# Optimization experiments

Hardware: AMD Instinct MI355X
Metric: run time of the kernel (lower is better)

The kernel has to match this reference:

```python
import jax, jax.numpy as jnp
import numpy as np

N_NODES = 200000


def _gcn_conv(x, W, b, src, dst, n):
    # PyG GCNConv: h = D^{-1/2} (A + I) D^{-1/2} (x @ W) + b
    h = x @ W  # [N, F_out]
    deg = jax.ops.segment_sum(jnp.ones(dst.shape[0], x.dtype), dst, num_segments=n)
    dinv = jnp.where(deg > 0, jax.lax.rsqrt(deg), 0.0)  # deg_inv_sqrt, inf -> 0
    norm = dinv[src] * dinv[dst]  # [E+N]
    msg = h[src] * norm[:, None]  # gather + scale, dominant memory traffic
    out = jax.ops.segment_sum(msg, dst, num_segments=n)
    return out + b


def setup_inputs() -> dict:
    key = jax.random.key(0)
    k1, k2, k3, k4, k5, k6 = jax.random.split(key, 6)
    x = jax.random.normal(k1, (N_NODES, 1), dtype=jnp.float32)
    edge_index = jax.random.randint(k2, (2, 12800000), 0, N_NODES, dtype=jnp.int64)
    # Glorot-style init like PyG GCNConv
    W1 = jax.random.normal(k3, (1, 16), dtype=jnp.float32) * (1.0 / np.sqrt(1))
    b1 = jnp.zeros((16,), dtype=jnp.float32)
    W2 = jax.random.normal(k4, (16, 1), dtype=jnp.float32) * (1.0 / np.sqrt(16))
    b2 = jnp.zeros((1,), dtype=jnp.float32)
    return {"x": x, "edge_index": edge_index, "W1": W1, "b1": b1, "W2": W2, "b2": b2}


def reference(x, edge_index, W1, b1, W2, b2):
    n = x.shape[0]
    # add self-loops once (static edge count: E + N)
    loops = jnp.arange(n, dtype=edge_index.dtype)
    src = jnp.concatenate([edge_index[0], loops])
    dst = jnp.concatenate([edge_index[1], loops])
    h = _gcn_conv(x, W1, b1, src, dst, n)
    h = jax.nn.relu(h)
    out = _gcn_conv(h, W2, b2, src, dst, n)
    return out
```

## Files before the change

kernel.cpp:

```cpp
#include <hip/hip_runtime.h>

#define TPB 256
#define BTPB 1024
#define STPB 512
#define LOG_S 13
#define S (1 << LOG_S)
#define RMAX 32
#define CHUNK 8192
#define MAXC 40
#define SLACK 32768
#define SCALEF 2097152.0f
#define INV_SCALEF (1.0f / 2097152.0f)


__global__ void k_initcur(int* __restrict__ cur, int R, int cap) {
    int t = threadIdx.x;
    if (t < R) cur[t] = t * cap;
}

__device__ inline int mbcnt64(unsigned long long m) {
    return __builtin_amdgcn_mbcnt_hi((unsigned)(m >> 32),
           __builtin_amdgcn_mbcnt_lo((unsigned)m, 0u));
}

__global__ __launch_bounds__(BTPB) void k_bin(const int* __restrict__ dst,
                                              const int* __restrict__ src, int e,
                                              int R, int cap,
                                              int* __restrict__ cur,
                                              unsigned* __restrict__ bkt) {
    __shared__ unsigned stage[CHUNK];
    __shared__ int h[RMAX], lofs[RMAX + 1], gbase[RMAX];
    int t = threadIdx.x;
    int b0 = blockIdx.x * CHUNK;
    int m = min(CHUNK, e - b0);
    if (t < RMAX) h[t] = 0;
    __syncthreads();
    unsigned pack[8];
    int rr[8];
    const int4* d4p = (const int4*)(dst + b0);
    const int4* s4p = (const int4*)(src + b0);
    int m4 = m >> 2;
    #pragma unroll
    for (int g = 0; g < 2; g++) {
        int i4 = g * BTPB + t;
        bool act = i4 < m4;
        int4 d = make_int4(0, 0, 0, 0), s = make_int4(0, 0, 0, 0);
        if (act) { d = d4p[i4]; s = s4p[i4]; }
        #pragma unroll
        for (int k = 0; k < 4; k++) {
            int dd = (k == 0) ? d.x : (k == 1) ? d.y : (k == 2) ? d.z : d.w;
            int ss = (k == 0) ? s.x : (k == 1) ? s.y : (k == 2) ? s.z : s.w;
            int r = act ? (dd >> LOG_S) : 31;
            unsigned long long m64 = ~0ull;
            #pragma unroll
            for (int b = 0; b < 5; b++) {
                unsigned long long vb = __ballot((r >> b) & 1);
                m64 &= ((r >> b) & 1) ? vb : ~vb;
            }
            int intra = mbcnt64(m64);
            int leader = __ffsll((long long)m64) - 1;
            int base = 0;
            if (intra == 0) base = atomicAdd(&h[r], __popcll(m64));
            base = __shfl(base, leader);
            int rk = base + intra;
            pack[g * 4 + k] = ((unsigned)(dd - (r << LOG_S)) << 18) | (unsigned)ss;
            rr[g * 4 + k] = act ? ((r << 13) | rk) : -1;
        }
    }
    __syncthreads();
    if (t < 64) {
        int hv = (t < R) ? h[t] : 0;
        int v = hv;
        for (int o = 1; o < 64; o <<= 1) {
            int u = __shfl_up(v, o);
            if (t >= o) v += u;
        }
        if (t < R) lofs[t] = v - hv;
        if (t == R - 1) lofs[R] = v;
        if (t < R && hv > 0) gbase[t] = atomicAdd(&cur[t], hv);
    }
    __syncthreads();
    #pragma unroll
    for (int k = 0; k < 8; k++) {
        if (rr[k] >= 0)
            stage[lofs[rr[k] >> 13] + (rr[k] & 8191)] = pack[k];
    }
    __syncthreads();
    for (int j = t; j < m; j += BTPB) {
        int lo = 0, hi = R;
        while (hi - lo > 1) {
            int mid = (lo + hi) >> 1;
            if (lofs[mid] <= j) lo = mid; else hi = mid;
        }
        int gi = gbase[lo] + (j - lofs[lo]);
        if (gi < (lo + 1) * cap)
            bkt[gi] = stage[j];
    }
}

template <int MODE>
__global__ __launch_bounds__(STPB) void k_scat(const unsigned* __restrict__ bkt,
                                               const int* __restrict__ cur,
                                               int cap,
                                               const float* __restrict__ val,
                                               int* __restrict__ partials, int bpr) {
    __shared__ int acc[S];
    int t = threadIdx.x;
    int r = blockIdx.x / bpr;
    int c = blockIdx.x - r * bpr;
    int4* acc4 = (int4*)acc;
    for (int j = t; j < S / 4; j += STPB) acc4[j] = make_int4(0, 0, 0, 0);
    __syncthreads();
    const unsigned* bk = bkt + (size_t)r * cap;
    int len = min(cur[r] - r * cap, cap);
    int len4 = len >> 2;
    const uint4* bk4 = (const uint4*)bk;
    int stride = bpr * STPB;
    int i0 = c * STPB + t;
    int i1 = i0 + stride;
    bool h0 = i0 < len4, h1 = i1 < len4;
    uint4 p0, p1;
    if (h0) p0 = bk4[i0];
    if (h1) p1 = bk4[i1];
    int inext = i0 + 2 * stride;
    while (h0) {
        uint4 p2;
        bool h2 = inext < len4;
        if (h2) p2 = bk4[inext];
        if (MODE == 0) {
            atomicAdd(&acc[p0.x >> 18], 1);
            atomicAdd(&acc[p0.y >> 18], 1);
            atomicAdd(&acc[p0.z >> 18], 1);
            atomicAdd(&acc[p0.w >> 18], 1);
        } else {
            atomicAdd(&acc[p0.x >> 18], (int)rintf(val[p0.x & 0x3FFFFu] * SCALEF));
            atomicAdd(&acc[p0.y >> 18], (int)rintf(val[p0.y & 0x3FFFFu] * SCALEF));
            atomicAdd(&acc[p0.z >> 18], (int)rintf(val[p0.z & 0x3FFFFu] * SCALEF));
            atomicAdd(&acc[p0.w >> 18], (int)rintf(val[p0.w & 0x3FFFFu] * SCALEF));
        }
        p0 = p1; h0 = h1;
        p1 = p2; h1 = h2;
        inext += stride;
    }
    for (int k = (len4 << 2) + c * STPB + t; k < len; k += stride) {
        unsigned p = bk[k];
        if (MODE == 0) atomicAdd(&acc[p >> 18], 1);
        else atomicAdd(&acc[p >> 18], (int)rintf(val[p & 0x3FFFFu] * SCALEF));
    }
    __syncthreads();
    int4* out4 = (int4*)(partials + (size_t)blockIdx.x * S);
    for (int j = t; j < S / 4; j += STPB) out4[j] = acc4[j];
}

__device__ inline int redp(const int* __restrict__ partials, int i, int bpr) {
    int r = i >> LOG_S;
    int slot = i & (S - 1);
    const int* p = partials + (size_t)r * bpr * S + slot;
    int s = 0;
    #pragma unroll 8
    for (int c = 0; c < bpr; c++) s += p[(size_t)c * S];
    return s;
}

__global__ void k_red_dinv(const int* __restrict__ partials, int bpr,
                           const float* __restrict__ x, float* __restrict__ dinv,
                           float* __restrict__ y, int n) {
    int i = blockIdx.x * blockDim.x + threadIdx.x;
    if (i < n) {
        float deg = (float)redp(partials, i, bpr) + 1.0f;
        float d = rsqrtf(deg);
        dinv[i] = d;
        y[i] = x[i] * d;
    }
}

__global__ void k_red_node(const int* __restrict__ partials, int bpr,
                           const float* __restrict__ dinv, const float* __restrict__ y,
                           float* __restrict__ z,
                           const float* __restrict__ W1, const float* __restrict__ b1,
                           const float* __restrict__ W2, int n, int f) {
    int i = blockIdx.x * blockDim.x + threadIdx.x;
    if (i < n) {
        float num = (float)redp(partials, i, bpr) * INV_SCALEF;
        float agg = dinv[i] * (num + y[i]);
        float h2 = 0.0f;
        for (int j = 0; j < f; j++) {
            float h = W1[j] * agg + b1[j];
            h2 += fmaxf(h, 0.0f) * W2[j];
        }
        z[i] = h2 * dinv[i];
    }
}

__global__ void k_red_out(const int* __restrict__ partials, int bpr,
                          const float* __restrict__ dinv, const float* __restrict__ z,
                          const float* __restrict__ b2, float* __restrict__ out, int n) {
    int i = blockIdx.x * blockDim.x + threadIdx.x;
    if (i < n) {
        float num = (float)redp(partials, i, bpr) * INV_SCALEF;
        out[i] = dinv[i] * (num + z[i]) + b2[0];
    }
}

__global__ void g_init(float* __restrict__ deg, float* __restrict__ num, int n) {
    int i = blockIdx.x * blockDim.x + threadIdx.x;
    if (i < n) { deg[i] = 1.0f; num[i] = 0.0f; }
}
__global__ void g_deg(const int* __restrict__ dst, float* __restrict__ deg, int e) {
    int i = blockIdx.x * blockDim.x + threadIdx.x;
    if (i < e) atomicAdd(deg + dst[i], 1.0f);
}
__global__ void g_dinv(const float* __restrict__ x, float* __restrict__ dd,
                       float* __restrict__ y, int n) {
    int i = blockIdx.x * blockDim.x + threadIdx.x;
    if (i < n) { float d = rsqrtf(dd[i]); dd[i] = d; y[i] = x[i] * d; }
}
__global__ void g_scatter(const int* __restrict__ src, const int* __restrict__ dst,
                          const float* __restrict__ val, float* __restrict__ num, int e) {
    int i = blockIdx.x * blockDim.x + threadIdx.x;
    if (i < e) atomicAdd(num + dst[i], val[src[i]]);
}
__global__ void g_node(const float* __restrict__ dinv, const float* __restrict__ y,
                       float* __restrict__ num, float* __restrict__ z,
                       const float* __restrict__ W1, const float* __restrict__ b1,
                       const float* __restrict__ W2, int n, int f) {
    int i = blockIdx.x * blockDim.x + threadIdx.x;
    if (i < n) {
        float agg = dinv[i] * (num[i] + y[i]);
        float h2 = 0.0f;
        for (int j = 0; j < f; j++) {
            float h = W1[j] * agg + b1[j];
            h2 += fmaxf(h, 0.0f) * W2[j];
        }
        z[i] = h2 * dinv[i];
        num[i] = 0.0f;
    }
}
__global__ void g_out(const float* __restrict__ dinv, const float* __restrict__ z,
                      const float* __restrict__ num, const float* __restrict__ b2,
                      float* __restrict__ out, int n) {
    int i = blockIdx.x * blockDim.x + threadIdx.x;
    if (i < n) out[i] = dinv[i] * (num[i] + z[i]) + b2[0];
}

extern "C" void kernel_launch(void* const* d_in, const int* in_sizes, int n_in,
                              void* d_out, int out_size, void* d_ws, size_t ws_size,
                              hipStream_t stream) {
    const float* x  = (const float*)d_in[0];
    const int*   ei = (const int*)d_in[1];
    const float* W1 = (const float*)d_in[2];
    const float* b1 = (const float*)d_in[3];
    const float* W2 = (const float*)d_in[4];
    const float* b2 = (const float*)d_in[5];

    int n = in_sizes[0];
    int e = in_sizes[1] / 2;
    int f = in_sizes[2];

    const int* src = ei;
    const int* dst = ei + e;
    float* out = (float*)d_out;

    int R  = (n + S - 1) >> LOG_S;
    int gn = (n + TPB - 1) / TPB;
    size_t words = ws_size / 4;

    size_t o_A   = 0;
    size_t o_B   = o_A + n;
    size_t o_D   = o_B + n;
    size_t o_cur = o_D + n;
    size_t o_bkt = (o_cur + RMAX + 3) & ~(size_t)3;
    int cap = ((e / R) + SLACK + 3) & ~3;
    size_t bkt_w = (size_t)R * cap;
    size_t o_part = o_bkt + bkt_w;

    float* A = (float*)d_ws + o_A;
    float* B = (float*)d_ws + o_B;
    float* D = (float*)d_ws + o_D;
    int*   cur = (int*)d_ws + o_cur;

    int bpr = 0;
    if (R <= 31 && n <= (1 << 18) && words > o_part) {
        size_t per_c = (size_t)R * S;
        size_t m = (words - o_part) / per_c;
        bpr = (int)(m > MAXC ? MAXC : m);
        while (bpr > 0 && R * bpr > 1024) bpr--;
    }

    if (bpr >= 4) {
        unsigned* bkt = (unsigned*)d_ws + o_bkt;
        int* partials = (int*)d_ws + o_part;
        int gs = R * bpr;
        int gbin = (e + CHUNK - 1) / CHUNK;
        k_initcur<<<1, RMAX, 0, stream>>>(cur, R, cap);
        k_bin<<<gbin, BTPB, 0, stream>>>(dst, src, e, R, cap, cur, bkt);
        k_scat<0><<<gs, STPB, 0, stream>>>(bkt, cur, cap, nullptr, partials, bpr);
        k_red_dinv<<<gn, TPB, 0, stream>>>(partials, bpr, x, A, B, n);
        k_scat<1><<<gs, STPB, 0, stream>>>(bkt, cur, cap, B, partials, bpr);
        k_red_node<<<gn, TPB, 0, stream>>>(partials, bpr, A, B, D, W1, b1, W2, n, f);
        k_scat<1><<<gs, STPB, 0, stream>>>(bkt, cur, cap, D, partials, bpr);
        k_red_out<<<gn, TPB, 0, stream>>>(partials, bpr, A, D, b2, out, n);
    } else {
        float* C = D + n;
        int ge = (e + TPB - 1) / TPB;
        g_init<<<gn, TPB, 0, stream>>>(A, C, n);
        g_deg<<<ge, TPB, 0, stream>>>(dst, A, e);
        g_dinv<<<gn, TPB, 0, stream>>>(x, A, B, n);
        g_scatter<<<ge, TPB, 0, stream>>>(src, dst, B, C, e);
        g_node<<<gn, TPB, 0, stream>>>(A, B, C, D, W1, b1, W2, n, f);
        g_scatter<<<ge, TPB, 0, stream>>>(src, dst, D, C, e);
        g_out<<<gn, TPB, 0, stream>>>(A, D, C, b2, out, n);
    }
}
```

Before: 333.9 us.

## Fold degree counting into binning via global atomics; drop wave-aggregated LDS ranking

Degree counting moves out of a separate bucket-scan pass and into the binning kernel, which now does a global atomicAdd per edge on a per-node degree array. The dinv reduction reads that array directly instead of summing per-block partials. The ballot-based wave-level aggregation of per-bucket LDS ranks is replaced by one plain LDS atomic per edge. This removes one full pass over the bucket array plus a partial reduction, but adds 12.8M random global atomics and more LDS atomic contention on a few hot bucket counters.

```diff
diff --git a/kernel.cpp b/kernel.cpp
--- a/kernel.cpp
+++ b/kernel.cpp
@@ -13,21 +13,19 @@
 #define INV_SCALEF (1.0f / 2097152.0f)
 
 
-__global__ void k_initcur(int* __restrict__ cur, int R, int cap) {
-    int t = threadIdx.x;
-    if (t < R) cur[t] = t * cap;
-}
-
-__device__ inline int mbcnt64(unsigned long long m) {
-    return __builtin_amdgcn_mbcnt_hi((unsigned)(m >> 32),
-           __builtin_amdgcn_mbcnt_lo((unsigned)m, 0u));
+__global__ void k_init(int* __restrict__ gdeg, int n, int* __restrict__ cur,
+                       int R, int cap) {
+    int i = blockIdx.x * blockDim.x + threadIdx.x;
+    if (i < n) gdeg[i] = 0;
+    if (blockIdx.x == 0 && threadIdx.x < R) cur[threadIdx.x] = threadIdx.x * cap;
 }
 
 __global__ __launch_bounds__(BTPB) void k_bin(const int* __restrict__ dst,
                                               const int* __restrict__ src, int e,
                                               int R, int cap,
                                               int* __restrict__ cur,
-                                              unsigned* __restrict__ bkt) {
+                                              unsigned* __restrict__ bkt,
+                                              int* __restrict__ gdeg) {
     __shared__ unsigned stage[CHUNK];
     __shared__ int h[RMAX], lofs[RMAX + 1], gbase[RMAX];
     int t = threadIdx.x;
@@ -43,28 +41,22 @@
     #pragma unroll
     for (int g = 0; g < 2; g++) {
         int i4 = g * BTPB + t;
-        bool act = i4 < m4;
-        int4 d = make_int4(0, 0, 0, 0), s = make_int4(0, 0, 0, 0);
-        if (act) { d = d4p[i4]; s = s4p[i4]; }
-        #pragma unroll
-        for (int k = 0; k < 4; k++) {
-            int dd = (k == 0) ? d.x : (k == 1) ? d.y : (k == 2) ? d.z : d.w;
-            int ss = (k == 0) ? s.x : (k == 1) ? s.y : (k == 2) ? s.z : s.w;
-            int r = act ? (dd >> LOG_S) : 31;
-            unsigned long long m64 = ~0ull;
+        if (i4 < m4) {
+            int4 d = d4p[i4];
+            int4 s = s4p[i4];
             #pragma unroll
-            for (int b = 0; b < 5; b++) {
-                unsigned long long vb = __ballot((r >> b) & 1);
-                m64 &= ((r >> b) & 1) ? vb : ~vb;
+            for (int k = 0; k < 4; k++) {
+                int dd = (k == 0) ? d.x : (k == 1) ? d.y : (k == 2) ? d.z : d.w;
+                int ss = (k == 0) ? s.x : (k == 1) ? s.y : (k == 2) ? s.z : s.w;
+                int r = dd >> LOG_S;
+                atomicAdd(&gdeg[dd], 1);
+                pack[g * 4 + k] = ((unsigned)(dd - (r << LOG_S)) << 18) | (unsigned)ss;
+                int rk = atomicAdd(&h[r], 1);
+                rr[g * 4 + k] = (r << 13) | rk;
             }
-            int intra = mbcnt64(m64);
-            int leader = __ffsll((long long)m64) - 1;
-            int base = 0;
-            if (intra == 0) base = atomicAdd(&h[r], __popcll(m64));
-            base = __shfl(base, leader);
-            int rk = base + intra;
-            pack[g * 4 + k] = ((unsigned)(dd - (r << LOG_S)) << 18) | (unsigned)ss;
-            rr[g * 4 + k] = act ? ((r << 13) | rk) : -1;
+        } else {
+            #pragma unroll
+            for (int k = 0; k < 4; k++) rr[g * 4 + k] = -1;
         }
     }
     __syncthreads();
@@ -98,7 +90,6 @@
     }
 }
 
-template <int MODE>
 __global__ __launch_bounds__(STPB) void k_scat(const unsigned* __restrict__ bkt,
                                                const int* __restrict__ cur,
                                                int cap,
@@ -127,32 +118,24 @@
         uint4 p2;
         bool h2 = inext < len4;
         if (h2) p2 = bk4[inext];
-        if (MODE == 0) {
-            atomicAdd(&acc[p0.x >> 18], 1);
-            atomicAdd(&acc[p0.y >> 18], 1);
-            atomicAdd(&acc[p0.z >> 18], 1);
-            atomicAdd(&acc[p0.w >> 18], 1);
-        } else {
-            atomicAdd(&acc[p0.x >> 18], (int)rintf(val[p0.x & 0x3FFFFu] * SCALEF));
-            atomicAdd(&acc[p0.y >> 18], (int)rintf(val[p0.y & 0x3FFFFu] * SCALEF));
-            atomicAdd(&acc[p0.z >> 18], (int)rintf(val[p0.z & 0x3FFFFu] * SCALEF));
-            atomicAdd(&acc[p0.w >> 18], (int)rintf(val[p0.w & 0x3FFFFu] * SCALEF));
-        }
+        atomicAdd(&acc[p0.x >> 18], (int)rintf(val[p0.x & 0x3FFFFu] * SCALEF));
+        atomicAdd(&acc[p0.y >> 18], (int)rintf(val[p0.y & 0x3FFFFu] * SCALEF));
+        atomicAdd(&acc[p0.z >> 18], (int)rintf(val[p0.z & 0x3FFFFu] * SCALEF));
+        atomicAdd(&acc[p0.w >> 18], (int)rintf(val[p0.w & 0x3FFFFu] * SCALEF));
         p0 = p1; h0 = h1;
         p1 = p2; h1 = h2;
         inext += stride;
     }
     for (int k = (len4 << 2) + c * STPB + t; k < len; k += stride) {
         unsigned p = bk[k];
-        if (MODE == 0) atomicAdd(&acc[p >> 18], 1);
-        else atomicAdd(&acc[p >> 18], (int)rintf(val[p & 0x3FFFFu] * SCALEF));
+        atomicAdd(&acc[p >> 18], (int)rintf(val[p & 0x3FFFFu] * SCALEF));
     }
     __syncthreads();
     int4* out4 = (int4*)(partials + (size_t)blockIdx.x * S);
     for (int j = t; j < S / 4; j += STPB) out4[j] = acc4[j];
 }
 
-__device__ inline int redp(const int* __restrict__ partials, int i, int bpr) {
+__device__ __forceinline__ int redp(const int* __restrict__ partials, int i, int bpr) {
     int r = i >> LOG_S;
     int slot = i & (S - 1);
     const int* p = partials + (size_t)r * bpr * S + slot;
@@ -162,12 +145,12 @@
     return s;
 }
 
-__global__ void k_red_dinv(const int* __restrict__ partials, int bpr,
+__global__ void k_red_dinv(const int* __restrict__ gdeg,
                            const float* __restrict__ x, float* __restrict__ dinv,
                            float* __restrict__ y, int n) {
     int i = blockIdx.x * blockDim.x + threadIdx.x;
     if (i < n) {
-        float deg = (float)redp(partials, i, bpr) + 1.0f;
+        float deg = (float)gdeg[i] + 1.0f;
         float d = rsqrtf(deg);
         dinv[i] = d;
         y[i] = x[i] * d;
@@ -269,7 +252,8 @@
     size_t o_B   = o_A + n;
     size_t o_D   = o_B + n;
     size_t o_cur = o_D + n;
-    size_t o_bkt = (o_cur + RMAX + 3) & ~(size_t)3;
+    size_t o_deg = o_cur + RMAX;
+    size_t o_bkt = (o_deg + n + 3) & ~(size_t)3;
     int cap = ((e / R) + SLACK + 3) & ~3;
     size_t bkt_w = (size_t)R * cap;
     size_t o_part = o_bkt + bkt_w;
@@ -278,9 +262,10 @@
     float* B = (float*)d_ws + o_B;
     float* D = (float*)d_ws + o_D;
     int*   cur = (int*)d_ws + o_cur;
+    int*   gdeg = (int*)d_ws + o_deg;
 
     int bpr = 0;
-    if (R <= 31 && n <= (1 << 18) && words > o_part) {
+    if (R <= RMAX && n <= (1 << 18) && words > o_part) {
         size_t per_c = (size_t)R * S;
         size_t m = (words - o_part) / per_c;
         bpr = (int)(m > MAXC ? MAXC : m);
@@ -292,13 +277,12 @@
         int* partials = (int*)d_ws + o_part;
         int gs = R * bpr;
         int gbin = (e + CHUNK - 1) / CHUNK;
-        k_initcur<<<1, RMAX, 0, stream>>>(cur, R, cap);
-        k_bin<<<gbin, BTPB, 0, stream>>>(dst, src, e, R, cap, cur, bkt);
-        k_scat<0><<<gs, STPB, 0, stream>>>(bkt, cur, cap, nullptr, partials, bpr);
-        k_red_dinv<<<gn, TPB, 0, stream>>>(partials, bpr, x, A, B, n);
-        k_scat<1><<<gs, STPB, 0, stream>>>(bkt, cur, cap, B, partials, bpr);
+        k_init<<<gn, TPB, 0, stream>>>(gdeg, n, cur, R, cap);
+        k_bin<<<gbin, BTPB, 0, stream>>>(dst, src, e, R, cap, cur, bkt, gdeg);
+        k_red_dinv<<<gn, TPB, 0, stream>>>(gdeg, x, A, B, n);
+        k_scat<<<gs, STPB, 0, stream>>>(bkt, cur, cap, B, partials, bpr);
         k_red_node<<<gn, TPB, 0, stream>>>(partials, bpr, A, B, D, W1, b1, W2, n, f);
-        k_scat<1><<<gs, STPB, 0, stream>>>(bkt, cur, cap, D, partials, bpr);
+        k_scat<<<gs, STPB, 0, stream>>>(bkt, cur, cap, D, partials, bpr);
         k_red_out<<<gn, TPB, 0, stream>>>(partials, bpr, A, D, b2, out, n);
     } else {
         float* C = D + n;
```

New measurement: 764.5 us. 2.29x slower.
